# Optimization experiments

Hardware: AMD Instinct MI355X
Metric: run time of the kernel (lower is better)

Reference implementation:

```python
import jax, jax.numpy as jnp
import numpy as np


def setup_inputs() -> dict:
    key = jax.random.key(0)
    k1, k2, k3 = jax.random.split(key, 3)
    B, Tc, Tq, D = 8, 4096, 1024, 256
    context = jax.random.normal(k1, (B, Tc, D), dtype=jnp.float32)
    question = jax.random.normal(k2, (B, Tq, D), dtype=jnp.float32)
    w = jax.random.normal(k3, (3 * D, 1), dtype=jnp.float32) * 0.05
    return {"context": context, "question": question, "w": w}


def reference(context, question, w):
    # context: (B, Tc, D); question: (B, Tq, D); w: (3D, 1)
    D = context.shape[-1]
    w1, w2, w3 = w[:D, 0], w[D:2 * D, 0], w[2 * D:, 0]
    # Fused similarity: S[b,i,j] = w1.c_i + w2.q_j + w3.(c_i*q_j)
    # (mathematically identical to the tiled concat + linear score, but
    # avoids materializing the (B,Tc,Tq,3D) tensor)
    s_c = jnp.einsum('bid,d->bi', context, w1)              # (B, Tc)
    s_q = jnp.einsum('bjd,d->bj', question, w2)             # (B, Tq)
    s_cq = jnp.einsum('bid,bjd->bij', context * w3, question)  # (B, Tc, Tq)
    S = s_cq + s_c[:, :, None] + s_q[:, None, :]
    A = jax.nn.softmax(S, axis=-1)                           # (B, Tc, Tq)
    # C2Q attention: U[b,i] = sum_j A[b,i,j] * q_j
    U = jnp.einsum('bij,bjd->bid', A, question)              # (B, Tc, D)
    # Q2C attention: b_i = max_j A[b,i,j]; h = sum_i b_i * c_i, tiled over Tc
    b = jnp.max(A, axis=-1)                                  # (B, Tc)
    h = jnp.einsum('bi,bid->bd', b, context)                 # (B, D)
    H = jnp.broadcast_to(h[:, None, :], context.shape)       # (B, Tc, D)
    # megamerge
    G = jnp.concatenate([context, U, context * U, context * H], axis=-1)
    return G  # (B, Tc, 4D)
```

## Files before the change

kernel.cpp:

```cpp
#include <hip/hip_runtime.h>
#include <hip/hip_bf16.h>
#include <stdint.h>
#include <stddef.h>


#define NB 8
#define TC 4096
#define TQ 1024
#define DD 256
#define JT 32
#define NJT (TQ / JT)

typedef __attribute__((ext_vector_type(4)))  float  f32x4v;
typedef __attribute__((ext_vector_type(8)))  __bf16 bf16x8v;
typedef __attribute__((ext_vector_type(4)))  __bf16 bf16x4v;

#define QA_OFF   0
#define QX_OFF   (QA_OFF + NB*NJT*16*1024)
#define SQ_OFF   (QX_OFF + NB*NJT*16*1024)
#define BV_OFF   (SQ_OFF + NB*TQ*4)
#define HV_OFF   (BV_OFF + NB*TC*4)

__device__ __forceinline__ void async_cp16(const void* g, void* l) {
  __builtin_amdgcn_global_load_lds(
      (const __attribute__((address_space(1))) void*)g,
      (__attribute__((address_space(3))) void*)l, 16, 0, 0);
}

__global__ __launch_bounds__(256) void k_qprep(const float* __restrict__ question,
                                               const float* __restrict__ w,
                                               char* __restrict__ ws) {
  uint4* qa = (uint4*)(ws + QA_OFF);
  uint4* qx = (uint4*)(ws + QX_OFF);
  float* sq = (float*)(ws + SQ_OFF);
  __shared__ __align__(16) __bf16 T[32][264];

  int bx = blockIdx.x;
  int b = bx >> 5, it = bx & 31;
  int t = threadIdx.x;
  int j = t >> 3;
  int seg = t & 7;

  const float* qrow = question + ((size_t)(b * TQ + it * JT + j)) * DD + seg * 32;
  const float* w2 = w + DD;

  float part = 0.f;
#pragma unroll
  for (int k = 0; k < 8; ++k) {
    float4 v  = *(const float4*)(qrow + 4 * k);
    float4 wv = *(const float4*)(w2 + seg * 32 + 4 * k);
    part += v.x * wv.x + v.y * wv.y + v.z * wv.z + v.w * wv.w;
    bf16x4v pk = {(__bf16)v.x, (__bf16)v.y, (__bf16)v.z, (__bf16)v.w};
    *(bf16x4v*)&T[j][seg * 32 + 4 * k] = pk;
  }
  part += __shfl_xor(part, 1);
  part += __shfl_xor(part, 2);
  part += __shfl_xor(part, 4);
  if (seg == 0) sq[b * TQ + it * JT + j] = part;
  __syncthreads();

#pragma unroll
  for (int p = 0; p < 4; ++p) {
    int ch = t + 256 * p;
    int L = ch & 63, cc = ch >> 6;
    int jm = cc >> 3, c = cc & 7;
    int nh = L & 15, qh = L >> 4;
    uint4 v = *(const uint4*)&T[16 * jm + nh][32 * c + 8 * qh];
    qa[(size_t)(b * NJT + it) * 1024 + ch] = v;
  }
#pragma unroll
  for (int p = 0; p < 4; ++p) {
    int ch = t + 256 * p;
    int L = ch & 63, mt = ch >> 6;
    int nh = L & 15, qh = L >> 4;
    __bf16 e[8];
#pragma unroll
    for (int o = 0; o < 8; ++o) e[o] = T[8 * qh + o][16 * mt + nh];
    qx[(size_t)(b * NJT + it) * 1024 + ch] = *(const uint4*)e;
  }
}

__global__ __launch_bounds__(256, 2) void k_main(const float* __restrict__ context,
                                                 const float* __restrict__ w,
                                                 const char* __restrict__ ws,
                                                 float* __restrict__ bv_out,
                                                 float* __restrict__ out) {
  const uint4*  qa = (const uint4*)(ws + QA_OFF);
  const __bf16* qx = (const __bf16*)(ws + QX_OFF);
  const float*  sq = (const float*)(ws + SQ_OFF);

  __shared__ __align__(16) __bf16 qa_lds[2][8192];
  __shared__ __align__(16) __bf16 pa_lds[4][16][40];
  __shared__ __align__(16) float  sq_all[TQ];
  __shared__ __align__(16) float  rinv_lds[64];

  int bx = blockIdx.x;
  int b = bx & 7;
  int ig = bx >> 3;
  int t = threadIdx.x;
  int wv = t >> 6;
  int lane = t & 63;
  int nh = lane & 15;
  int qh = lane >> 4;
  int i0w = ig * 64 + wv * 16;

  const uint4* qa_b = qa + (size_t)b * NJT * 1024;
  const __bf16* qx_b = qx + (size_t)b * NJT * 8192;
  const float* sqb = sq + b * TQ;

  bf16x8v cw3f[8];
  {
    const float* crow = context + ((size_t)(b * TC + i0w + nh)) * DD;
    const float* w3 = w + 2 * DD;
#pragma unroll
    for (int c = 0; c < 8; ++c) {
      int d0 = 32 * c + 8 * qh;
      float4 f0 = *(const float4*)(crow + d0);
      float4 f1 = *(const float4*)(crow + d0 + 4);
      float4 g0 = *(const float4*)(w3 + d0);
      float4 g1 = *(const float4*)(w3 + d0 + 4);
      bf16x8v fr;
      fr[0] = (__bf16)(f0.x * g0.x); fr[1] = (__bf16)(f0.y * g0.y);
      fr[2] = (__bf16)(f0.z * g0.z); fr[3] = (__bf16)(f0.w * g0.w);
      fr[4] = (__bf16)(f1.x * g1.x); fr[5] = (__bf16)(f1.y * g1.y);
      fr[6] = (__bf16)(f1.z * g1.z); fr[7] = (__bf16)(f1.w * g1.w);
      cw3f[c] = fr;
    }
  }

  {
    ((float4*)sq_all)[t] = ((const float4*)sqb)[t];
    const uint4* src = qa_b;
#pragma unroll
    for (int p = 0; p < 4; ++p) {
      int cb = wv * 64 + p * 256;
      async_cp16(src + cb + lane, &qa_lds[0][(size_t)cb * 8]);
    }
  }

  f32x4v U[16];
#pragma unroll
  for (int k = 0; k < 16; ++k) U[k] = (f32x4v){0.f, 0.f, 0.f, 0.f};
  float m_run = -1e30f, l_run = 0.f;

  __syncthreads();

  for (int itq = 0; itq < NJT; ++itq) {
    int cur = itq & 1;

    if (itq + 1 < NJT) {
      const uint4* src = qa_b + (size_t)(itq + 1) * 1024;
#pragma unroll
      for (int p = 0; p < 4; ++p) {
        int cb = wv * 64 + p * 256;
        async_cp16(src + cb + lane, &qa_lds[cur ^ 1][(size_t)cb * 8]);
      }
    }

    f32x4v S0 = {0.f, 0.f, 0.f, 0.f}, S1 = {0.f, 0.f, 0.f, 0.f};
#pragma unroll
    for (int c = 0; c < 8; ++c) {
      bf16x8v a0 = *(const bf16x8v*)&qa_lds[cur][((0 * 8 + c) * 64 + lane) * 8];
      bf16x8v a1 = *(const bf16x8v*)&qa_lds[cur][((1 * 8 + c) * 64 + lane) * 8];
      S0 = __builtin_amdgcn_mfma_f32_16x16x32_bf16(a0, cw3f[c], S0, 0, 0, 0);
      S1 = __builtin_amdgcn_mfma_f32_16x16x32_bf16(a1, cw3f[c], S1, 0, 0, 0);
    }

    bf16x8v bqr[4];
    {
      const __bf16* qxt = qx_b + (size_t)itq * 8192 + lane * 8;
#pragma unroll
      for (int nt = 0; nt < 4; ++nt)
        bqr[nt] = *(const bf16x8v*)(qxt + (size_t)(wv * 4 + nt) * 512);
    }

    float4 sq0 = *(const float4*)&sq_all[itq * JT + 4 * qh];
    float4 sq1 = *(const float4*)&sq_all[itq * JT + 16 + 4 * qh];
    float e0 = __expf(S0[0] + sq0.x), e1 = __expf(S0[1] + sq0.y);
    float e2 = __expf(S0[2] + sq0.z), e3 = __expf(S0[3] + sq0.w);
    float f0 = __expf(S1[0] + sq1.x), f1 = __expf(S1[1] + sq1.y);
    float f2 = __expf(S1[2] + sq1.z), f3 = __expf(S1[3] + sq1.w);
    float v0 = fmaxf(fmaxf(S0[0] + sq0.x, S0[1] + sq0.y), fmaxf(S0[2] + sq0.z, S0[3] + sq0.w));
    float v1 = fmaxf(fmaxf(S1[0] + sq1.x, S1[1] + sq1.y), fmaxf(S1[2] + sq1.z, S1[3] + sq1.w));
    m_run = fmaxf(m_run, fmaxf(v0, v1));
    l_run += ((e0 + e1) + (e2 + e3)) + ((f0 + f1) + (f2 + f3));

    bf16x4v pk0 = {(__bf16)e0, (__bf16)e1, (__bf16)e2, (__bf16)e3};
    bf16x4v pk1 = {(__bf16)f0, (__bf16)f1, (__bf16)f2, (__bf16)f3};
    *(bf16x4v*)&pa_lds[wv][nh][4 * qh]      = pk0;
    *(bf16x4v*)&pa_lds[wv][nh][16 + 4 * qh] = pk1;

    asm volatile("s_waitcnt lgkmcnt(0)\n\ts_barrier" ::: "memory");

#pragma unroll
    for (int mi = 0; mi < 4; ++mi) {
      bf16x8v af = *(const bf16x8v*)&pa_lds[mi][nh][8 * qh];
#pragma unroll
      for (int nt = 0; nt < 4; ++nt)
        U[mi * 4 + nt] = __builtin_amdgcn_mfma_f32_16x16x32_bf16(af, bqr[nt], U[mi * 4 + nt], 0, 0, 0);
    }

    __syncthreads();
  }

  float lo = l_run + __shfl_xor(l_run, 16);
  lo += __shfl_xor(lo, 32);
  float mo = fmaxf(m_run, __shfl_xor(m_run, 16));
  mo = fmaxf(mo, __shfl_xor(mo, 32));
  float rinv = 1.0f / lo;
  if (lane < 16) {
    bv_out[b * TC + i0w + nh] = __expf(mo) * rinv;
    rinv_lds[wv * 16 + nh] = rinv;
  }
  __syncthreads();

#pragma unroll
  for (int mi = 0; mi < 4; ++mi) {
#pragma unroll
    for (int r = 0; r < 4; ++r) {
      int row = ig * 64 + mi * 16 + 4 * qh + r;
      float rv = rinv_lds[mi * 16 + 4 * qh + r];
      const float* crow = context + ((size_t)(b * TC + row)) * DD;
      float* orow = out + ((size_t)(b * TC + row)) * (4 * DD);
#pragma unroll
      for (int nt = 0; nt < 4; ++nt) {
        int d = wv * 64 + nt * 16 + nh;
        float c = crow[d];
        float u = U[mi * 4 + nt][r] * rv;
        orow[d] = c;
        orow[DD + d] = u;
        orow[2 * DD + d] = c * u;
      }
    }
  }
}

__global__ __launch_bounds__(256) void k_hred(const float* __restrict__ context,
                                              const char* __restrict__ ws,
                                              float* __restrict__ hv) {
  const float* bv = (const float*)(ws + BV_OFF);
  __shared__ float bsh[128];
  int bx = blockIdx.x;
  int b = bx >> 5, ch = bx & 31;
  int i0 = ch * 128;
  int t = threadIdx.x;
  if (t < 128) bsh[t] = bv[b * TC + i0 + t];
  __syncthreads();
  float acc = 0.f;
  const float* cp = context + ((size_t)(b * TC + i0)) * DD + t;
#pragma unroll 4
  for (int r = 0; r < 128; ++r) acc += bsh[r] * cp[(size_t)r * DD];
  atomicAdd(&hv[b * DD + t], acc);
}

__global__ __launch_bounds__(256) void k_final(const float* __restrict__ context,
                                               const char* __restrict__ ws,
                                               float* __restrict__ out) {
  const float* hv = (const float*)(ws + HV_OFF);
  int gid = blockIdx.x * 256 + threadIdx.x;
  int row = gid >> 6;
  int d = (gid & 63) * 4;
  int b = row >> 12;
  float4 c4 = ((const float4*)context)[gid];
  float4 h4 = *(const float4*)(hv + b * DD + d);
  float4 r;
  r.x = c4.x * h4.x; r.y = c4.y * h4.y; r.z = c4.z * h4.z; r.w = c4.w * h4.w;
  *(float4*)(out + (size_t)row * TQ + 3 * DD + d) = r;
}

extern "C" void kernel_launch(void* const* d_in, const int* in_sizes, int n_in,
                              void* d_out, int out_size, void* d_ws, size_t ws_size,
                              hipStream_t stream) {
  (void)in_sizes; (void)n_in; (void)out_size; (void)ws_size;
  const float* context  = (const float*)d_in[0];
  const float* question = (const float*)d_in[1];
  const float* w        = (const float*)d_in[2];
  float* out = (float*)d_out;
  char* ws = (char*)d_ws;

  k_qprep<<<NB * NJT, 256, 0, stream>>>(question, w, ws);
  k_main<<<NB * (TC / 64), 256, 0, stream>>>(context, w, ws,
                                             (float*)(ws + BV_OFF), out);
  hipMemsetAsync(ws + HV_OFF, 0, NB * DD * sizeof(float), stream);
  k_hred<<<NB * 32, 256, 0, stream>>>(context, ws, (float*)(ws + HV_OFF));
  k_final<<<(NB * TC * DD / 4) / 256, 256, 0, stream>>>(context, ws, out);
}
```

Measured before the change: 225.0 us.

## Fuse Q2C h-reduction into main kernel and split S tiles across waves 2x2

Removes the separate k_hred kernel and the bv workspace round-trip. Each main block now accumulates b_i*c_i in its epilogue and atomically adds the partial sums into hv. The S computation is also repartitioned: waves form a 2x2 grid over row-tiles and j-halves, so each wave reuses one LDS A-fragment for two row tiles. This halves LDS reads for S, and a cross-wave reduction of the softmax sums and maxima is added in its place. The trade-off is more atomics (one per block per column), extra registers for the second context fragment set, and a second barrier in the epilogue.

```diff
diff --git a/kernel.cpp b/kernel.cpp
--- a/kernel.cpp
+++ b/kernel.cpp
@@ -18,8 +18,7 @@
 #define QA_OFF   0
 #define QX_OFF   (QA_OFF + NB*NJT*16*1024)
 #define SQ_OFF   (QX_OFF + NB*NJT*16*1024)
-#define BV_OFF   (SQ_OFF + NB*TQ*4)
-#define HV_OFF   (BV_OFF + NB*TC*4)
+#define HV_OFF   (SQ_OFF + NB*TQ*4)
 
 __device__ __forceinline__ void async_cp16(const void* g, void* l) {
   __builtin_amdgcn_global_load_lds(
@@ -83,7 +82,7 @@
 __global__ __launch_bounds__(256, 2) void k_main(const float* __restrict__ context,
                                                  const float* __restrict__ w,
                                                  const char* __restrict__ ws,
-                                                 float* __restrict__ bv_out,
+                                                 float* __restrict__ hv,
                                                  float* __restrict__ out) {
   const uint4*  qa = (const uint4*)(ws + QA_OFF);
   const __bf16* qx = (const __bf16*)(ws + QX_OFF);
@@ -92,7 +91,9 @@
   __shared__ __align__(16) __bf16 qa_lds[2][8192];
   __shared__ __align__(16) __bf16 pa_lds[4][16][40];
   __shared__ __align__(16) float  sq_all[TQ];
+  __shared__ __align__(16) float  red_lm[2][4][16][2];
   __shared__ __align__(16) float  rinv_lds[64];
+  __shared__ __align__(16) float  bvv_lds[64];
 
   int bx = blockIdx.x;
   int b = bx & 7;
@@ -100,31 +101,42 @@
   int t = threadIdx.x;
   int wv = t >> 6;
   int lane = t & 63;
+  int wi = wv >> 1;
+  int wj = wv & 1;
+  int it0 = 2 * wi, it1 = 2 * wi + 1;
   int nh = lane & 15;
   int qh = lane >> 4;
-  int i0w = ig * 64 + wv * 16;
 
   const uint4* qa_b = qa + (size_t)b * NJT * 1024;
   const __bf16* qx_b = qx + (size_t)b * NJT * 8192;
   const float* sqb = sq + b * TQ;
 
-  bf16x8v cw3f[8];
+  bf16x8v cw3f0[8], cw3f1[8];
   {
-    const float* crow = context + ((size_t)(b * TC + i0w + nh)) * DD;
+    const float* crow0 = context + ((size_t)(b * TC + ig * 64 + 32 * wi + nh)) * DD;
+    const float* crow1 = crow0 + 16 * DD;
     const float* w3 = w + 2 * DD;
 #pragma unroll
     for (int c = 0; c < 8; ++c) {
       int d0 = 32 * c + 8 * qh;
-      float4 f0 = *(const float4*)(crow + d0);
-      float4 f1 = *(const float4*)(crow + d0 + 4);
       float4 g0 = *(const float4*)(w3 + d0);
       float4 g1 = *(const float4*)(w3 + d0 + 4);
+      float4 f0 = *(const float4*)(crow0 + d0);
+      float4 f1 = *(const float4*)(crow0 + d0 + 4);
       bf16x8v fr;
       fr[0] = (__bf16)(f0.x * g0.x); fr[1] = (__bf16)(f0.y * g0.y);
       fr[2] = (__bf16)(f0.z * g0.z); fr[3] = (__bf16)(f0.w * g0.w);
       fr[4] = (__bf16)(f1.x * g1.x); fr[5] = (__bf16)(f1.y * g1.y);
       fr[6] = (__bf16)(f1.z * g1.z); fr[7] = (__bf16)(f1.w * g1.w);
-      cw3f[c] = fr;
+      cw3f0[c] = fr;
+      float4 h0 = *(const float4*)(crow1 + d0);
+      float4 h1 = *(const float4*)(crow1 + d0 + 4);
+      bf16x8v hr;
+      hr[0] = (__bf16)(h0.x * g0.x); hr[1] = (__bf16)(h0.y * g0.y);
+      hr[2] = (__bf16)(h0.z * g0.z); hr[3] = (__bf16)(h0.w * g0.w);
+      hr[4] = (__bf16)(h1.x * g1.x); hr[5] = (__bf16)(h1.y * g1.y);
+      hr[6] = (__bf16)(h1.z * g1.z); hr[7] = (__bf16)(h1.w * g1.w);
+      cw3f1[c] = hr;
     }
   }
 
@@ -141,12 +153,21 @@
   f32x4v U[16];
 #pragma unroll
   for (int k = 0; k < 16; ++k) U[k] = (f32x4v){0.f, 0.f, 0.f, 0.f};
-  float m_run = -1e30f, l_run = 0.f;
+  float m0_run = -1e30f, l0_run = 0.f;
+  float m1_run = -1e30f, l1_run = 0.f;
 
   __syncthreads();
 
   for (int itq = 0; itq < NJT; ++itq) {
     int cur = itq & 1;
+
+    bf16x8v bqr[4];
+    {
+      const __bf16* qxt = qx_b + (size_t)itq * 8192 + lane * 8;
+#pragma unroll
+      for (int nt = 0; nt < 4; ++nt)
+        bqr[nt] = *(const bf16x8v*)(qxt + (size_t)(wv * 4 + nt) * 512);
+    }
 
     if (itq + 1 < NJT) {
       const uint4* src = qa_b + (size_t)(itq + 1) * 1024;
@@ -160,35 +181,25 @@
     f32x4v S0 = {0.f, 0.f, 0.f, 0.f}, S1 = {0.f, 0.f, 0.f, 0.f};
 #pragma unroll
     for (int c = 0; c < 8; ++c) {
-      bf16x8v a0 = *(const bf16x8v*)&qa_lds[cur][((0 * 8 + c) * 64 + lane) * 8];
-      bf16x8v a1 = *(const bf16x8v*)&qa_lds[cur][((1 * 8 + c) * 64 + lane) * 8];
-      S0 = __builtin_amdgcn_mfma_f32_16x16x32_bf16(a0, cw3f[c], S0, 0, 0, 0);
-      S1 = __builtin_amdgcn_mfma_f32_16x16x32_bf16(a1, cw3f[c], S1, 0, 0, 0);
-    }
-
-    bf16x8v bqr[4];
-    {
-      const __bf16* qxt = qx_b + (size_t)itq * 8192 + lane * 8;
-#pragma unroll
-      for (int nt = 0; nt < 4; ++nt)
-        bqr[nt] = *(const bf16x8v*)(qxt + (size_t)(wv * 4 + nt) * 512);
-    }
-
-    float4 sq0 = *(const float4*)&sq_all[itq * JT + 4 * qh];
-    float4 sq1 = *(const float4*)&sq_all[itq * JT + 16 + 4 * qh];
-    float e0 = __expf(S0[0] + sq0.x), e1 = __expf(S0[1] + sq0.y);
-    float e2 = __expf(S0[2] + sq0.z), e3 = __expf(S0[3] + sq0.w);
-    float f0 = __expf(S1[0] + sq1.x), f1 = __expf(S1[1] + sq1.y);
-    float f2 = __expf(S1[2] + sq1.z), f3 = __expf(S1[3] + sq1.w);
-    float v0 = fmaxf(fmaxf(S0[0] + sq0.x, S0[1] + sq0.y), fmaxf(S0[2] + sq0.z, S0[3] + sq0.w));
-    float v1 = fmaxf(fmaxf(S1[0] + sq1.x, S1[1] + sq1.y), fmaxf(S1[2] + sq1.z, S1[3] + sq1.w));
-    m_run = fmaxf(m_run, fmaxf(v0, v1));
-    l_run += ((e0 + e1) + (e2 + e3)) + ((f0 + f1) + (f2 + f3));
+      bf16x8v ac = *(const bf16x8v*)&qa_lds[cur][((wj * 8 + c) * 64 + lane) * 8];
+      S0 = __builtin_amdgcn_mfma_f32_16x16x32_bf16(ac, cw3f0[c], S0, 0, 0, 0);
+      S1 = __builtin_amdgcn_mfma_f32_16x16x32_bf16(ac, cw3f1[c], S1, 0, 0, 0);
+    }
+
+    float4 sqv = *(const float4*)&sq_all[itq * JT + 16 * wj + 4 * qh];
+    float a0 = S0[0] + sqv.x, a1 = S0[1] + sqv.y, a2 = S0[2] + sqv.z, a3 = S0[3] + sqv.w;
+    float b0 = S1[0] + sqv.x, b1 = S1[1] + sqv.y, b2 = S1[2] + sqv.z, b3 = S1[3] + sqv.w;
+    float e0 = __expf(a0), e1 = __expf(a1), e2 = __expf(a2), e3 = __expf(a3);
+    float f0 = __expf(b0), f1 = __expf(b1), f2 = __expf(b2), f3 = __expf(b3);
+    m0_run = fmaxf(m0_run, fmaxf(fmaxf(a0, a1), fmaxf(a2, a3)));
+    m1_run = fmaxf(m1_run, fmaxf(fmaxf(b0, b1), fmaxf(b2, b3)));
+    l0_run += (e0 + e1) + (e2 + e3);
+    l1_run += (f0 + f1) + (f2 + f3);
 
     bf16x4v pk0 = {(__bf16)e0, (__bf16)e1, (__bf16)e2, (__bf16)e3};
     bf16x4v pk1 = {(__bf16)f0, (__bf16)f1, (__bf16)f2, (__bf16)f3};
-    *(bf16x4v*)&pa_lds[wv][nh][4 * qh]      = pk0;
-    *(bf16x4v*)&pa_lds[wv][nh][16 + 4 * qh] = pk1;
+    *(bf16x4v*)&pa_lds[it0][nh][16 * wj + 4 * qh] = pk0;
+    *(bf16x4v*)&pa_lds[it1][nh][16 * wj + 4 * qh] = pk1;
 
     asm volatile("s_waitcnt lgkmcnt(0)\n\ts_barrier" ::: "memory");
 
@@ -203,23 +214,34 @@
     __syncthreads();
   }
 
-  float lo = l_run + __shfl_xor(l_run, 16);
-  lo += __shfl_xor(lo, 32);
-  float mo = fmaxf(m_run, __shfl_xor(m_run, 16));
-  mo = fmaxf(mo, __shfl_xor(mo, 32));
-  float rinv = 1.0f / lo;
+  float lo0 = l0_run + __shfl_xor(l0_run, 16); lo0 += __shfl_xor(lo0, 32);
+  float lo1 = l1_run + __shfl_xor(l1_run, 16); lo1 += __shfl_xor(lo1, 32);
+  float mo0 = fmaxf(m0_run, __shfl_xor(m0_run, 16)); mo0 = fmaxf(mo0, __shfl_xor(mo0, 32));
+  float mo1 = fmaxf(m1_run, __shfl_xor(m1_run, 16)); mo1 = fmaxf(mo1, __shfl_xor(mo1, 32));
   if (lane < 16) {
-    bv_out[b * TC + i0w + nh] = __expf(mo) * rinv;
-    rinv_lds[wv * 16 + nh] = rinv;
-  }
-  __syncthreads();
-
+    red_lm[wj][it0][nh][0] = lo0; red_lm[wj][it0][nh][1] = mo0;
+    red_lm[wj][it1][nh][0] = lo1; red_lm[wj][it1][nh][1] = mo1;
+  }
+  __syncthreads();
+  if (t < 64) {
+    int it = t >> 4, n = t & 15;
+    float l = red_lm[0][it][n][0] + red_lm[1][it][n][0];
+    float m = fmaxf(red_lm[0][it][n][1], red_lm[1][it][n][1]);
+    float ri = 1.0f / l;
+    rinv_lds[t] = ri;
+    bvv_lds[t] = __expf(m) * ri;
+  }
+  __syncthreads();
+
+  float hacc[4] = {0.f, 0.f, 0.f, 0.f};
 #pragma unroll
   for (int mi = 0; mi < 4; ++mi) {
 #pragma unroll
     for (int r = 0; r < 4; ++r) {
-      int row = ig * 64 + mi * 16 + 4 * qh + r;
-      float rv = rinv_lds[mi * 16 + 4 * qh + r];
+      int rl = mi * 16 + 4 * qh + r;
+      int row = ig * 64 + rl;
+      float rv = rinv_lds[rl];
+      float bb = bvv_lds[rl];
       const float* crow = context + ((size_t)(b * TC + row)) * DD;
       float* orow = out + ((size_t)(b * TC + row)) * (4 * DD);
 #pragma unroll
@@ -230,27 +252,16 @@
         orow[d] = c;
         orow[DD + d] = u;
         orow[2 * DD + d] = c * u;
+        hacc[nt] += bb * c;
       }
     }
   }
-}
-
-__global__ __launch_bounds__(256) void k_hred(const float* __restrict__ context,
-                                              const char* __restrict__ ws,
-                                              float* __restrict__ hv) {
-  const float* bv = (const float*)(ws + BV_OFF);
-  __shared__ float bsh[128];
-  int bx = blockIdx.x;
-  int b = bx >> 5, ch = bx & 31;
-  int i0 = ch * 128;
-  int t = threadIdx.x;
-  if (t < 128) bsh[t] = bv[b * TC + i0 + t];
-  __syncthreads();
-  float acc = 0.f;
-  const float* cp = context + ((size_t)(b * TC + i0)) * DD + t;
-#pragma unroll 4
-  for (int r = 0; r < 128; ++r) acc += bsh[r] * cp[(size_t)r * DD];
-  atomicAdd(&hv[b * DD + t], acc);
+#pragma unroll
+  for (int nt = 0; nt < 4; ++nt) {
+    float h = hacc[nt] + __shfl_xor(hacc[nt], 16);
+    h += __shfl_xor(h, 32);
+    if (qh == 0) atomicAdd(&hv[b * DD + wv * 64 + nt * 16 + nh], h);
+  }
 }
 
 __global__ __launch_bounds__(256) void k_final(const float* __restrict__ context,
@@ -279,9 +290,8 @@
   char* ws = (char*)d_ws;
 
   k_qprep<<<NB * NJT, 256, 0, stream>>>(question, w, ws);
+  hipMemsetAsync(ws + HV_OFF, 0, NB * DD * sizeof(float), stream);
   k_main<<<NB * (TC / 64), 256, 0, stream>>>(context, w, ws,
-                                             (float*)(ws + BV_OFF), out);
-  hipMemsetAsync(ws + HV_OFF, 0, NB * DD * sizeof(float), stream);
-  k_hred<<<NB * 32, 256, 0, stream>>>(context, ws, (float*)(ws + HV_OFF));
+                                             (float*)(ws + HV_OFF), out);
   k_final<<<(NB * TC * DD / 4) / 256, 256, 0, stream>>>(context, ws, out);
 }
```

Result: faster. 212.6 us (-5.5%).
